# Performance work log

Hardware: AMD Instinct MI355X
Metric: run time of the kernel (lower is better)

## Reference

```python
import jax, jax.numpy as jnp
import numpy as np

# dims: batch, seqlen, d_model, d_inner=2*d_model, d_state, dt_rank=ceil(dm/16), n_layer, vocab, d_conv
B_, L_, DM, DI, N, RK, NL, V, K = 2, 2048, 512, 1024, 16, 32, 4, 32000, 4


def setup_inputs() -> dict:
    key = jax.random.key(0)
    ks = jax.random.split(key, 10)
    s = lambda k, shape, scale: jax.random.normal(k, shape, jnp.float32) * scale
    return {
        "input_ids": jax.random.randint(ks[0], (B_, L_), 0, V),
        "emb": s(ks[1], (V, DM), 0.02),
        "in_proj_w": s(ks[2], (NL, 2 * DI, DM), DM ** -0.5),
        "conv_w": s(ks[3], (NL, DI, K), 0.2),
        "conv_b": jnp.zeros((NL, DI), jnp.float32),
        "x_proj_w": s(ks[4], (NL, RK + 2 * N, DI), DI ** -0.5),
        "dt_proj_w": s(ks[5], (NL, DI, RK), RK ** -0.5),
        "dt_proj_b": jnp.full((NL, DI), -4.6, jnp.float32),  # softplus^-1(~0.01)
        "A_log": jnp.tile(jnp.log(jnp.arange(1, N + 1, dtype=jnp.float32))[None, None, :], (NL, DI, 1)),
        "Dp": jnp.ones((NL, DI), jnp.float32),
        "out_proj_w": s(ks[6], (NL, DM, DI), DI ** -0.5),
        "norm_w": jnp.ones((NL, DM), jnp.float32),
        "norm_b": jnp.zeros((NL, DM), jnp.float32),
        "normf_w": jnp.ones((DM,), jnp.float32),
        "normf_b": jnp.zeros((DM,), jnp.float32),
        "dec_w": s(ks[7], (V, DM), DM ** -0.5),
        "dec_b": jnp.zeros((V,), jnp.float32),
    }


def layer_norm(x, w, b, eps=1e-5):
    m = x.mean(-1, keepdims=True)
    v = ((x - m) ** 2).mean(-1, keepdims=True)
    return (x - m) * jax.lax.rsqrt(v + eps) * w + b


def mamba_mixer(x, iw, cw, cb, xw, dw, db, A_log, Dv, ow):
    B, L, _ = x.shape
    xz = x @ iw.T                      # [B,L,2*DI]
    u, z = jnp.split(xz, 2, -1)
    # depthwise causal conv1d, kernel K
    up = jnp.pad(u, ((0, 0), (K - 1, 0), (0, 0)))
    u = sum(up[:, k:k + L, :] * cw[:, k] for k in range(K)) + cb
    u = jax.nn.silu(u)
    xdbl = u @ xw.T                    # [B,L,RK+2N]
    dt, Bm, Cm = jnp.split(xdbl, [RK, RK + N], -1)
    dt = jax.nn.softplus(dt @ dw.T + db)   # [B,L,DI]
    A = -jnp.exp(A_log)                    # [DI,N]
    dA = jnp.exp(dt[..., None] * A)                              # [B,L,DI,N]
    dBu = dt[..., None] * Bm[:, :, None, :] * u[..., None]       # [B,L,DI,N]

    def step(h, inp):
        dA_t, dBu_t, C_t = inp
        h = dA_t * h + dBu_t
        return h, jnp.einsum('bdn,bn->bd', h, C_t)

    h0 = jnp.zeros((B, DI, N), x.dtype)
    _, ys = jax.lax.scan(step, h0, (dA.transpose(1, 0, 2, 3), dBu.transpose(1, 0, 2, 3), Cm.transpose(1, 0, 2)))
    y = ys.transpose(1, 0, 2) + u * Dv
    y = y * jax.nn.silu(z)
    return y @ ow.T


def reference(input_ids, emb, in_proj_w, conv_w, conv_b, x_proj_w, dt_proj_w, dt_proj_b,
              A_log, Dp, out_proj_w, norm_w, norm_b, normf_w, normf_b, dec_w, dec_b):
    h = emb[input_ids]                 # [B,L,DM]
    residual = None
    for i in range(NL):
        residual = h + residual if residual is not None else h
        hn = layer_norm(residual, norm_w[i], norm_b[i])
        h = mamba_mixer(hn, in_proj_w[i], conv_w[i], conv_b[i], x_proj_w[i],
                        dt_proj_w[i], dt_proj_b[i], A_log[i], Dp[i], out_proj_w[i])
    residual = h + residual
    h = layer_norm(residual, normf_w, normf_b)
    return h @ dec_w.T + dec_b         # [B,L,V]
```

## Files before the change

kernel.cpp:

```cpp
#include <hip/hip_runtime.h>
#include <cstdint>
#include <cstddef>

typedef unsigned short u16;
typedef __attribute__((ext_vector_type(8))) short short8;
typedef __attribute__((ext_vector_type(4))) float f32x4;
typedef __attribute__((ext_vector_type(4))) unsigned short us4;

#define NB 2
#define SEQ 2048
#define DMODEL 512
#define DINNER 1024
#define NSTATE 16
#define RKK 32
#define NLAYER 4
#define VOCAB 32000
#define MROWS 4096
#define NCHUNK 128
#define LCHUNK 16
#define XP_SPLITK 4
#define XP_KCH 256

#define GLOAD16(gp, lp) __builtin_amdgcn_global_load_lds( \
    (const __attribute__((address_space(1))) void*)(gp),  \
    (__attribute__((address_space(3))) void*)(lp), 16, 0, 0)

static __device__ __forceinline__ u16 f2bf(float f) {
  union { float f; uint32_t u; } v; v.f = f;
  uint32_t r = (v.u + 0x7FFFu + ((v.u >> 16) & 1u)) >> 16;
  return (u16)r;
}
static __device__ __forceinline__ float bf2f(u16 x) {
  union { uint32_t u; float f; } v; v.u = ((uint32_t)x) << 16; return v.f;
}

__global__ __launch_bounds__(256) void cvt_all_k(
    const float* __restrict__ ipw, const float* __restrict__ dtw,
    const float* __restrict__ opw, const float* __restrict__ dw,
    const float* __restrict__ xpw,
    u16* __restrict__ w_in, u16* __restrict__ w_dt,
    u16* __restrict__ w_out, u16* __restrict__ w_dec,
    u16* __restrict__ w_xp) {
  const long n0 = (long)NLAYER * 2 * DINNER * DMODEL / 4;
  const long n1 = (long)NLAYER * DINNER * RKK / 4;
  const long n2 = (long)NLAYER * DMODEL * DINNER / 4;
  const long n3 = (long)VOCAB * DMODEL / 4;
  const long n4 = (long)NLAYER * 128 * DINNER / 4;
  long i = (long)blockIdx.x * 256 + threadIdx.x;
  if (i >= n0 + n1 + n2 + n3 + n4) return;
  if (i >= n0 + n1 + n2 + n3) {
    long o4 = (i - n0 - n1 - n2 - n3) * 4;
    int c = (int)(o4 & 1023); int r = ((int)(o4 >> 10)) & 127; int l = (int)(o4 >> 17);
    us4 o;
    if (r < 64) {
      f32x4 v = *(const f32x4*)(xpw + (((long)l * 64 + r) << 10) + c);
      o.x = f2bf(v.x); o.y = f2bf(v.y); o.z = f2bf(v.z); o.w = f2bf(v.w);
    } else { o.x = 0; o.y = 0; o.z = 0; o.w = 0; }
    *(us4*)(w_xp + o4) = o;
    return;
  }
  const float* s; u16* d; long off;
  if (i < n0) { s = ipw; d = w_in; off = i; }
  else if (i < n0 + n1) { s = dtw; d = w_dt; off = i - n0; }
  else if (i < n0 + n1 + n2) { s = opw; d = w_out; off = i - n0 - n1; }
  else { s = dw; d = w_dec; off = i - n0 - n1 - n2; }
  f32x4 v = *(const f32x4*)(s + off * 4);
  us4 o; o.x = f2bf(v.x); o.y = f2bf(v.y); o.z = f2bf(v.z); o.w = f2bf(v.w);
  *(us4*)(d + off * 4) = o;
}

template <int MODE>
__global__ __launch_bounds__(256) void ln_k(const int* __restrict__ ids, const float* __restrict__ emb,
                                            float* __restrict__ resid, const float* __restrict__ h0,
                                            const float* __restrict__ h1,
                                            const float* __restrict__ w, const float* __restrict__ b,
                                            u16* __restrict__ obf) {
  int m = blockIdx.x, t = threadIdx.x;
  long base = (long)m * DMODEL;
  float x0, x1;
  if (MODE == 0) {
    long ebase = (long)ids[m] * DMODEL;
    x0 = emb[ebase + t]; x1 = emb[ebase + t + 256];
    resid[base + t] = x0; resid[base + t + 256] = x1;
  } else {
    x0 = resid[base + t] + h0[base + t] + h1[base + t];
    x1 = resid[base + t + 256] + h0[base + t + 256] + h1[base + t + 256];
    resid[base + t] = x0; resid[base + t + 256] = x1;
  }
  float s = x0 + x1, q = x0 * x0 + x1 * x1;
  #pragma unroll
  for (int o = 1; o < 64; o <<= 1) { s += __shfl_xor(s, o, 64); q += __shfl_xor(q, o, 64); }
  __shared__ float ss[4], qq[4];
  int wv = t >> 6;
  if ((t & 63) == 0) { ss[wv] = s; qq[wv] = q; }
  __syncthreads();
  s = ss[0] + ss[1] + ss[2] + ss[3];
  q = qq[0] + qq[1] + qq[2] + qq[3];
  float mean = s * (1.f / DMODEL);
  float var = q * (1.f / DMODEL) - mean * mean;
  float rs = rsqrtf(var + 1e-5f);
  obf[base + t]       = f2bf((x0 - mean) * rs * w[t] + b[t]);
  obf[base + t + 256] = f2bf((x1 - mean) * rs * w[t + 256] + b[t + 256]);
}

__global__ __launch_bounds__(256) void conv_silu_k(const u16* __restrict__ xzb, const float* __restrict__ cw,
                            const float* __restrict__ cb, u16* __restrict__ ub) {
  int tid = blockIdx.x * 256 + threadIdx.x;
  int d = tid & (DINNER - 1);
  int g = tid >> 10;
  int m0 = g << 3;
  int t0 = m0 & (SEQ - 1);
  float w0 = cw[d * 4 + 0], w1 = cw[d * 4 + 1], w2 = cw[d * 4 + 2], w3 = cw[d * 4 + 3];
  float bias = cb[d];
  float v[11];
  #pragma unroll
  for (int j = 0; j < 11; ++j) {
    int tt = t0 + j - 3;
    v[j] = (tt >= 0) ? bf2f(xzb[(long)(m0 + j - 3) * (2 * DINNER) + d]) : 0.f;
  }
  #pragma unroll
  for (int i = 0; i < 8; ++i) {
    float acc = bias + v[i] * w0 + v[i + 1] * w1 + v[i + 2] * w2 + v[i + 3] * w3;
    float sv = acc / (1.f + __expf(-acc));
    ub[(long)(m0 + i) * DINNER + d] = f2bf(sv);
  }
}

template <int EPI, int BK, bool SPLIT>
__global__ __launch_bounds__(256) void gemm_bf16(
    const u16* __restrict__ A, int lda, const u16* __restrict__ W, int ldw,
    float* __restrict__ C, u16* __restrict__ Cb, int ldc,
    const float* __restrict__ bias, int K, int kchunk, long zstride) {
  const int tid = threadIdx.x;
  const int nwg = gridDim.x * gridDim.y;
  const int wgid = blockIdx.y * gridDim.x + blockIdx.x;
  const int q = nwg >> 3;
  const int swz = (wgid & 7) * q + (wgid >> 3);
  const int bn = swz % gridDim.x, bm = swz / gridDim.x;
  int kb = 0, ke = K;
  if (SPLIT) { kb = blockIdx.z * kchunk; ke = kb + kchunk; C += (long)blockIdx.z * zstride; }
  const int wave = tid >> 6, lane = tid & 63;
  const int wm = (wave >> 1) * 64, wn = (wave & 1) * 64;
  __shared__ __align__(16) u16 sA[128 * BK];
  __shared__ __align__(16) u16 sB[128 * BK];
  f32x4 acc[4][4] = {};
  const long arow0 = (long)bm * 128, brow0 = (long)bn * 128;
  const int frow = lane & 15, fk = (lane >> 4) << 3;
  const int rsw = (frow & 7) << 3;
  for (int k0 = kb; k0 < ke; k0 += BK) {
    __syncthreads();
    if (BK == 32) {
      const int srow = lane >> 2, scol = (lane & 3) << 3;
      #pragma unroll
      for (int i = 0; i < 2; ++i) {
        int c = wave * 2 + i;
        GLOAD16(A + (arow0 + 16 * c + srow) * (long)lda + k0 + scol, sA + c * 512);
        GLOAD16(W + (brow0 + 16 * c + srow) * (long)ldw + k0 + scol, sB + c * 512);
      }
    } else {
      const int srow = lane >> 3;
      const int scol = (((lane & 7) ^ (lane >> 3)) << 3);
      #pragma unroll
      for (int i = 0; i < 4; ++i) {
        int c = wave * 4 + i;
        GLOAD16(A + (arow0 + 8 * c + srow) * (long)lda + k0 + scol, sA + c * 512);
        GLOAD16(W + (brow0 + 8 * c + srow) * (long)ldw + k0 + scol, sB + c * 512);
      }
    }
    asm volatile("s_waitcnt vmcnt(0)" ::: "memory");
    __syncthreads();
    #pragma unroll
    for (int ks = 0; ks < BK / 32; ++ks) {
      short8 aF[4], bF[4];
      #pragma unroll
      for (int i = 0; i < 4; ++i) {
        int idx = (wm + i * 16 + frow) * BK + ks * 32 + fk;
        aF[i] = *(const short8*)(sA + (BK == 64 ? (idx ^ rsw) : idx));
      }
      #pragma unroll
      for (int i = 0; i < 4; ++i) {
        int idx = (wn + i * 16 + frow) * BK + ks * 32 + fk;
        bF[i] = *(const short8*)(sB + (BK == 64 ? (idx ^ rsw) : idx));
      }
      #pragma unroll
      for (int mi = 0; mi < 4; ++mi)
        #pragma unroll
        for (int ni = 0; ni < 4; ++ni)
          acc[mi][ni] = __builtin_amdgcn_mfma_f32_16x16x32_bf16(aF[mi], bF[ni], acc[mi][ni], 0, 0, 0);
    }
  }
  const int ccol = lane & 15, crow = (lane >> 4) << 2;
  #pragma unroll
  for (int mi = 0; mi < 4; ++mi) {
    #pragma unroll
    for (int ni = 0; ni < 4; ++ni) {
      long gr0 = arow0 + wm + mi * 16 + crow;
      long gc = brow0 + wn + ni * 16 + ccol;
      #pragma unroll
      for (int r = 0; r < 4; ++r) {
        float v = acc[mi][ni][r];
        long idx = (gr0 + r) * (long)ldc + gc;
        if (EPI == 0) {
          C[idx] = v;
        } else if (EPI == 1) {
          Cb[idx] = f2bf(v);
        } else if (EPI == 2) {
          float x = v + bias[gc];
          Cb[idx] = f2bf((x > 20.f) ? x : log1pf(__expf(x)));
        } else {
          __builtin_nontemporal_store(v + bias[gc], &C[idx]);
        }
      }
    }
  }
}

__global__ __launch_bounds__(512) void gemm_dec(
    const u16* __restrict__ A, const u16* __restrict__ W,
    float* __restrict__ C, const float* __restrict__ bias) {
  const int tid = threadIdx.x;
  const int nwg = gridDim.x * gridDim.y;
  const int wgid = blockIdx.y * gridDim.x + blockIdx.x;
  const int q = nwg >> 3;
  const int swz = (wgid & 7) * q + (wgid >> 3);
  const int bn = swz % gridDim.x, bm = swz / gridDim.x;
  const int wave = tid >> 6, lane = tid & 63;
  const int wm = (wave >> 1) << 6;
  const int wn = (wave & 1) << 6;
  __shared__ __align__(16) u16 sA[256 * 64];
  __shared__ __align__(16) u16 sB[128 * 64];
  f32x4 acc[4][4] = {};
  const long arow0 = (long)bm * 256, brow0 = (long)bn * 128;
  const int frow = lane & 15, fk = (lane >> 4) << 3;
  const int rsw = (frow & 7) << 3;
  const int srow = lane >> 3;
  const int scol = (((lane & 7) ^ (lane >> 3)) << 3);
  for (int k0 = 0; k0 < DMODEL; k0 += 64) {
    __syncthreads();
    #pragma unroll
    for (int i = 0; i < 4; ++i) {
      int c = wave * 4 + i;
      GLOAD16(A + (arow0 + 8 * c + srow) * (long)DMODEL + k0 + scol, sA + c * 512);
    }
    #pragma unroll
    for (int i = 0; i < 2; ++i) {
      int c = wave * 2 + i;
      GLOAD16(W + (brow0 + 8 * c + srow) * (long)DMODEL + k0 + scol, sB + c * 512);
    }
    asm volatile("s_waitcnt vmcnt(0)" ::: "memory");
    __syncthreads();
    #pragma unroll
    for (int ks = 0; ks < 2; ++ks) {
      short8 aF[4], bF[4];
      #pragma unroll
      for (int i = 0; i < 4; ++i) {
        int idx = (wm + i * 16 + frow) * 64 + ks * 32 + fk;
        aF[i] = *(const short8*)(sA + (idx ^ rsw));
      }
      #pragma unroll
      for (int i = 0; i < 4; ++i) {
        int idx = (wn + i * 16 + frow) * 64 + ks * 32 + fk;
        bF[i] = *(const short8*)(sB + (idx ^ rsw));
      }
      #pragma unroll
      for (int mi = 0; mi < 4; ++mi)
        #pragma unroll
        for (int ni = 0; ni < 4; ++ni)
          acc[mi][ni] = __builtin_amdgcn_mfma_f32_16x16x32_bf16(aF[mi], bF[ni], acc[mi][ni], 0, 0, 0);
    }
  }
  const int ccol = lane & 15, crow = (lane >> 4) << 2;
  #pragma unroll
  for (int mi = 0; mi < 4; ++mi) {
    #pragma unroll
    for (int ni = 0; ni < 4; ++ni) {
      long gr0 = arow0 + wm + mi * 16 + crow;
      long gc = brow0 + wn + ni * 16 + ccol;
      float bv = bias[gc];
      #pragma unroll
      for (int r = 0; r < 4; ++r)
        __builtin_nontemporal_store(acc[mi][ni][r] + bv, &C[(gr0 + r) * (long)VOCAB + gc]);
    }
  }
}

__global__ __launch_bounds__(256) void xp_comb_k(const float* __restrict__ P, float* __restrict__ xd,
                          u16* __restrict__ xdb) {
  long i = (long)blockIdx.x * 256 + threadIdx.x;
  int col = (int)(i & 127);
  if (col >= 64) return;
  float s = 0.f;
  #pragma unroll
  for (int z = 0; z < XP_SPLITK; ++z) s += P[(long)z * MROWS * 128 + i];
  if (col < 32) xdb[i] = f2bf(s);
  else xd[i] = s;
}

__global__ __launch_bounds__(256) void scanA_k(const u16* __restrict__ dtb, const u16* __restrict__ ubf,
                        const float* __restrict__ xd, const float* __restrict__ alog_l,
                        float* __restrict__ P, float* __restrict__ S) {
  int bid = blockIdx.x;
  int tid = threadIdx.x;
  int b = bid >> 9;
  int c = (bid >> 2) & (NCHUNK - 1);
  int d = ((bid & 3) << 8) + tid;
  long rbase = (long)(b * SEQ + c * LCHUNK);
  __shared__ __align__(16) float sB[LCHUNK][NSTATE];
  if (tid < 64) {
    int t = tid >> 2, k4 = (tid & 3) << 2;
    *(f32x4*)&sB[t][k4] = *(const f32x4*)(xd + (rbase + t) * 128 + RKK + k4);
  }
  u16 dtv[LCHUNK], uv[LCHUNK];
  const u16* dp = dtb + rbase * DINNER + d;
  const u16* up = ubf + rbase * DINNER + d;
  #pragma unroll
  for (int tt = 0; tt < LCHUNK; ++tt) { dtv[tt] = dp[(long)tt * DINNER]; uv[tt] = up[(long)tt * DINNER]; }
  float A[NSTATE], h[NSTATE];
  #pragma unroll
  for (int n4 = 0; n4 < 4; ++n4) {
    f32x4 a4 = *(const f32x4*)(alog_l + d * NSTATE + n4 * 4);
    #pragma unroll
    for (int j = 0; j < 4; ++j) { A[n4 * 4 + j] = -__expf(a4[j]); h[n4 * 4 + j] = 0.f; }
  }
  __syncthreads();
  float dsum = 0.f;
  #pragma unroll
  for (int tt = 0; tt < LCHUNK; ++tt) {
    float dv = bf2f(dtv[tt]);
    float du = dv * bf2f(uv[tt]);
    dsum += dv;
    f32x4 b0 = *(const f32x4*)&sB[tt][0], b1 = *(const f32x4*)&sB[tt][4];
    f32x4 b2 = *(const f32x4*)&sB[tt][8], b3 = *(const f32x4*)&sB[tt][12];
    #pragma unroll
    for (int n = 0; n < NSTATE; ++n) {
      float dA = __expf(dv * A[n]);
      float bx = (n < 4) ? b0[n & 3] : (n < 8) ? b1[n & 3] : (n < 12) ? b2[n & 3] : b3[n & 3];
      h[n] = dA * h[n] + du * bx;
    }
  }
  long base = (((long)(b * DINNER + d)) * NCHUNK + c) * NSTATE;
  #pragma unroll
  for (int n4 = 0; n4 < 4; ++n4) {
    f32x4 pv, sv;
    #pragma unroll
    for (int j = 0; j < 4; ++j) { pv[j] = __expf(A[n4 * 4 + j] * dsum); sv[j] = h[n4 * 4 + j]; }
    *(f32x4*)(P + base + n4 * 4) = pv;
    *(f32x4*)(S + base + n4 * 4) = sv;
  }
}

__global__ __launch_bounds__(256) void scanB_k(const float* __restrict__ P, const float* __restrict__ S,
                        float* __restrict__ Hin) {
  int w = blockIdx.x * 4 + (threadIdx.x >> 6);
  int lane = threadIdx.x & 63;
  long base0 = ((long)w * NCHUNK + 2 * lane) * NSTATE;
  long base1 = base0 + NSTATE;
  float p0[NSTATE], s0[NSTATE], p[NSTATE], s[NSTATE];
  #pragma unroll
  for (int n = 0; n < NSTATE; ++n) {
    p0[n] = P[base0 + n]; s0[n] = S[base0 + n];
    float p1 = P[base1 + n], s1 = S[base1 + n];
    p[n] = p1 * p0[n];
    s[n] = p1 * s0[n] + s1;
  }
  #pragma unroll
  for (int off = 1; off < 64; off <<= 1) {
    float pp[NSTATE], sp[NSTATE];
    #pragma unroll
    for (int n = 0; n < NSTATE; ++n) {
      pp[n] = __shfl_up(p[n], off, 64);
      sp[n] = __shfl_up(s[n], off, 64);
    }
    if (lane >= off) {
      #pragma unroll
      for (int n = 0; n < NSTATE; ++n) { s[n] = p[n] * sp[n] + s[n]; p[n] *= pp[n]; }
    }
  }
  #pragma unroll
  for (int n = 0; n < NSTATE; ++n) {
    float hv = __shfl_up(s[n], 1, 64);
    float e = (lane == 0) ? 0.f : hv;
    Hin[base0 + n] = e;
    Hin[base1 + n] = p0[n] * e + s0[n];
  }
}

__global__ __launch_bounds__(256) void scanC_k(const u16* __restrict__ dtb, const u16* __restrict__ ubf,
                        const float* __restrict__ xd, const float* __restrict__ alog_l,
                        const float* __restrict__ Dp_l, const u16* __restrict__ xzb,
                        const float* __restrict__ Hin, u16* __restrict__ ybf) {
  int bid = blockIdx.x;
  int tid = threadIdx.x;
  int b = bid >> 9;
  int c = (bid >> 2) & (NCHUNK - 1);
  int d = ((bid & 3) << 8) + tid;
  long rbase = (long)(b * SEQ + c * LCHUNK);
  __shared__ __align__(16) float sBC[LCHUNK][2 * NSTATE];
  if (tid < 128) {
    int t = tid >> 3, k4 = (tid & 7) << 2;
    *(f32x4*)&sBC[t][k4] = *(const f32x4*)(xd + (rbase + t) * 128 + RKK + k4);
  }
  u16 dtv[LCHUNK], uv[LCHUNK], zv[LCHUNK];
  const u16* dp = dtb + rbase * DINNER + d;
  const u16* up = ubf + rbase * DINNER + d;
  const u16* zp = xzb + rbase * (2 * DINNER) + DINNER + d;
  #pragma unroll
  for (int tt = 0; tt < LCHUNK; ++tt) {
    dtv[tt] = dp[(long)tt * DINNER]; uv[tt] = up[(long)tt * DINNER];
    zv[tt] = zp[(long)tt * 2 * DINNER];
  }
  float A[NSTATE], h[NSTATE];
  long hbase = (((long)(b * DINNER + d)) * NCHUNK + c) * NSTATE;
  #pragma unroll
  for (int n4 = 0; n4 < 4; ++n4) {
    f32x4 a4 = *(const f32x4*)(alog_l + d * NSTATE + n4 * 4);
    f32x4 h4 = *(const f32x4*)(Hin + hbase + n4 * 4);
    #pragma unroll
    for (int j = 0; j < 4; ++j) { A[n4 * 4 + j] = -__expf(a4[j]); h[n4 * 4 + j] = h4[j]; }
  }
  float Dv = Dp_l[d];
  u16* yp = ybf + rbase * DINNER + d;
  __syncthreads();
  #pragma unroll
  for (int tt = 0; tt < LCHUNK; ++tt) {
    float dv = bf2f(dtv[tt]);
    float uvf = bf2f(uv[tt]);
    float du = dv * uvf;
    f32x4 b0 = *(const f32x4*)&sBC[tt][0], b1 = *(const f32x4*)&sBC[tt][4];
    f32x4 b2 = *(const f32x4*)&sBC[tt][8], b3 = *(const f32x4*)&sBC[tt][12];
    f32x4 c0 = *(const f32x4*)&sBC[tt][16], c1 = *(const f32x4*)&sBC[tt][20];
    f32x4 c2 = *(const f32x4*)&sBC[tt][24], c3 = *(const f32x4*)&sBC[tt][28];
    float y = 0.f;
    #pragma unroll
    for (int n = 0; n < NSTATE; ++n) {
      float dA = __expf(dv * A[n]);
      float bx = (n < 4) ? b0[n & 3] : (n < 8) ? b1[n & 3] : (n < 12) ? b2[n & 3] : b3[n & 3];
      float cx = (n < 4) ? c0[n & 3] : (n < 8) ? c1[n & 3] : (n < 12) ? c2[n & 3] : c3[n & 3];
      h[n] = dA * h[n] + du * bx;
      y += h[n] * cx;
    }
    y += uvf * Dv;
    float z = bf2f(zv[tt]);
    y *= z / (1.f + __expf(-z));
    yp[(long)tt * DINNER] = f2bf(y);
  }
}

extern "C" void kernel_launch(void* const* d_in, const int* in_sizes, int n_in,
                              void* d_out, int out_size, void* d_ws, size_t ws_size,
                              hipStream_t stream) {
  (void)in_sizes; (void)n_in; (void)out_size; (void)ws_size;
  const int*   ids = (const int*)d_in[0];
  const float* emb = (const float*)d_in[1];
  const float* ipw = (const float*)d_in[2];
  const float* cw  = (const float*)d_in[3];
  const float* cb  = (const float*)d_in[4];
  const float* xpw = (const float*)d_in[5];
  const float* dtw = (const float*)d_in[6];
  const float* dtb = (const float*)d_in[7];
  const float* alg = (const float*)d_in[8];
  const float* Dpp = (const float*)d_in[9];
  const float* opw = (const float*)d_in[10];
  const float* nw  = (const float*)d_in[11];
  const float* nb  = (const float*)d_in[12];
  const float* nfw = (const float*)d_in[13];
  const float* nfb = (const float*)d_in[14];
  const float* dw  = (const float*)d_in[15];
  const float* db  = (const float*)d_in[16];

  char* p = (char*)d_ws;
  auto carve = [&](size_t bytes) { void* r = (void*)p; p += (bytes + 255) & ~(size_t)255; return r; };
  float* resid  = (float*)carve((size_t)MROWS * DMODEL * 4);
  float* hmixP  = (float*)carve((size_t)2 * MROWS * DMODEL * 4);
  u16*   hnbf   = (u16*)  carve((size_t)MROWS * DMODEL * 2);
  u16*   hfbf   = (u16*)  carve((size_t)MROWS * DMODEL * 2);
  u16*   xzb    = (u16*)  carve((size_t)MROWS * 2 * DINNER * 2);
  u16*   ubf    = (u16*)  carve((size_t)MROWS * DINNER * 2);
  float* xdbl   = (float*)carve((size_t)MROWS * 128 * 4);
  u16*   xdblbf = (u16*)  carve((size_t)MROWS * 128 * 2);
  float* xdP    = (float*)carve((size_t)XP_SPLITK * MROWS * 128 * 4);
  u16*   dtb16  = (u16*)  carve((size_t)MROWS * DINNER * 2);
  u16*   ybf    = (u16*)  carve((size_t)MROWS * DINNER * 2);
  float* chkP   = (float*)carve((size_t)NB * DINNER * NCHUNK * NSTATE * 4);
  float* chkS   = (float*)carve((size_t)NB * DINNER * NCHUNK * NSTATE * 4);
  float* hin    = (float*)carve((size_t)NB * DINNER * NCHUNK * NSTATE * 4);
  u16*   w_in   = (u16*)carve((size_t)NLAYER * 2 * DINNER * DMODEL * 2);
  u16*   w_xp   = (u16*)carve((size_t)NLAYER * 128 * DINNER * 2);
  u16*   w_dt   = (u16*)carve((size_t)NLAYER * DINNER * RKK * 2);
  u16*   w_out  = (u16*)carve((size_t)NLAYER * DMODEL * DINNER * 2);
  u16*   w_dec  = (u16*)carve((size_t)VOCAB * DMODEL * 2);

  {
    long nv = ((long)NLAYER * 2 * DINNER * DMODEL + (long)NLAYER * DINNER * RKK +
               (long)NLAYER * DMODEL * DINNER + (long)VOCAB * DMODEL +
               (long)NLAYER * 128 * DINNER) / 4;
    cvt_all_k<<<(int)((nv + 255) / 256), 256, 0, stream>>>(
        ipw, dtw, opw, dw, xpw, w_in, w_dt, w_out, w_dec, w_xp);
  }

  for (int i = 0; i < NLAYER; ++i) {
    if (i == 0)
      ln_k<0><<<MROWS, 256, 0, stream>>>(ids, emb, resid, nullptr, nullptr, nw, nb, hnbf);
    else
      ln_k<1><<<MROWS, 256, 0, stream>>>(nullptr, nullptr, resid, hmixP, hmixP + (long)MROWS * DMODEL,
                                         nw + i * DMODEL, nb + i * DMODEL, hnbf);
    gemm_bf16<1, 64, false><<<dim3(2 * DINNER / 128, MROWS / 128), 256, 0, stream>>>(
        hnbf, DMODEL, w_in + (long)i * 2 * DINNER * DMODEL, DMODEL,
        nullptr, xzb, 2 * DINNER, nullptr, DMODEL, 0, 0);
    conv_silu_k<<<(MROWS / 8 * DINNER) / 256, 256, 0, stream>>>(
        xzb, cw + (long)i * DINNER * 4, cb + i * DINNER, ubf);
    gemm_bf16<0, 64, true><<<dim3(1, MROWS / 128, XP_SPLITK), 256, 0, stream>>>(
        ubf, DINNER, w_xp + (long)i * 128 * DINNER, DINNER,
        xdP, nullptr, 128, nullptr, DINNER, XP_KCH, (long)MROWS * 128);
    xp_comb_k<<<(MROWS * 128) / 256, 256, 0, stream>>>(xdP, xdbl, xdblbf);
    gemm_bf16<2, 32, false><<<dim3(DINNER / 128, MROWS / 128), 256, 0, stream>>>(
        xdblbf, 128, w_dt + (long)i * DINNER * RKK, RKK,
        nullptr, dtb16, DINNER, dtb + i * DINNER, RKK, 0, 0);
    scanA_k<<<NB * NCHUNK * 4, 256, 0, stream>>>(
        dtb16, ubf, xdbl, alg + (long)i * DINNER * NSTATE, chkP, chkS);
    scanB_k<<<(NB * DINNER) / 4, 256, 0, stream>>>(chkP, chkS, hin);
    scanC_k<<<NB * NCHUNK * 4, 256, 0, stream>>>(
        dtb16, ubf, xdbl, alg + (long)i * DINNER * NSTATE, Dpp + i * DINNER, xzb, hin, ybf);
    gemm_bf16<0, 64, true><<<dim3(DMODEL / 128, MROWS / 128, 2), 256, 0, stream>>>(
        ybf, DINNER, w_out + (long)i * DMODEL * DINNER, DINNER,
        hmixP, nullptr, DMODEL, nullptr, DINNER, DINNER / 2, (long)MROWS * DMODEL);
  }
  ln_k<1><<<MROWS, 256, 0, stream>>>(nullptr, nullptr, resid, hmixP, hmixP + (long)MROWS * DMODEL,
                                     nfw, nfb, hfbf);
  gemm_dec<<<dim3(VOCAB / 128, MROWS / 256), 512, 0, stream>>>(
      hfbf, w_dec, (float*)d_out, db);
}
```

Measured before the change: 827.7 us.

## Double-buffer decoder GEMM, lengthen scan chunks, raise split-K for projections

The decoder GEMM now uses double-buffered shared-memory tiles with K-step 32, prefetching the next tile while MFMAs run on the current one instead of load-wait-compute per step. The scan moves to 64 chunks of 32 steps, so the cross-chunk combine in scanB handles one chunk per lane instead of pairing two. The x_proj split-K rises to 8 and out_proj split-K to 4, with the layer norm summing the extra partial buffers. This adds parallelism for the small GEMMs but costs more partial-sum traffic and longer sequential scan chunks.

Result: faster. 774.6 us (-6.4%).

```diff
diff --git a/kernel.cpp b/kernel.cpp
--- a/kernel.cpp
+++ b/kernel.cpp
@@ -16,10 +16,11 @@
 #define NLAYER 4
 #define VOCAB 32000
 #define MROWS 4096
-#define NCHUNK 128
-#define LCHUNK 16
-#define XP_SPLITK 4
-#define XP_KCH 256
+#define NCHUNK 64
+#define LCHUNK 32
+#define XP_SPLITK 8
+#define XP_KCH 128
+#define OUT_SPLITK 4
 
 #define GLOAD16(gp, lp) __builtin_amdgcn_global_load_lds( \
     (const __attribute__((address_space(1))) void*)(gp),  \
@@ -71,8 +72,8 @@
 
 template <int MODE>
 __global__ __launch_bounds__(256) void ln_k(const int* __restrict__ ids, const float* __restrict__ emb,
-                                            float* __restrict__ resid, const float* __restrict__ h0,
-                                            const float* __restrict__ h1,
+                                            float* __restrict__ resid, const float* __restrict__ hP,
+                                            long pstride,
                                             const float* __restrict__ w, const float* __restrict__ b,
                                             u16* __restrict__ obf) {
   int m = blockIdx.x, t = threadIdx.x;
@@ -83,8 +84,13 @@
     x0 = emb[ebase + t]; x1 = emb[ebase + t + 256];
     resid[base + t] = x0; resid[base + t + 256] = x1;
   } else {
-    x0 = resid[base + t] + h0[base + t] + h1[base + t];
-    x1 = resid[base + t + 256] + h0[base + t + 256] + h1[base + t + 256];
+    x0 = resid[base + t];
+    x1 = resid[base + t + 256];
+    #pragma unroll
+    for (int z = 0; z < OUT_SPLITK; ++z) {
+      x0 += hP[z * pstride + base + t];
+      x1 += hP[z * pstride + base + t + 256];
+    }
     resid[base + t] = x0; resid[base + t + 256] = x1;
   }
   float s = x0 + x1, q = x0 * x0 + x1 * x1;
@@ -227,47 +233,51 @@
   const int wave = tid >> 6, lane = tid & 63;
   const int wm = (wave >> 1) << 6;
   const int wn = (wave & 1) << 6;
-  __shared__ __align__(16) u16 sA[256 * 64];
-  __shared__ __align__(16) u16 sB[128 * 64];
+  __shared__ __align__(16) u16 sA[2][256 * 32];
+  __shared__ __align__(16) u16 sB[2][128 * 32];
   f32x4 acc[4][4] = {};
   const long arow0 = (long)bm * 256, brow0 = (long)bn * 128;
   const int frow = lane & 15, fk = (lane >> 4) << 3;
-  const int rsw = (frow & 7) << 3;
-  const int srow = lane >> 3;
-  const int scol = (((lane & 7) ^ (lane >> 3)) << 3);
-  for (int k0 = 0; k0 < DMODEL; k0 += 64) {
-    __syncthreads();
+  const int srow = lane >> 2;
+  const int scol = (((lane & 3) ^ (srow & 3)) << 3);
+  #pragma unroll
+  for (int i = 0; i < 2; ++i) {
+    int c = wave * 2 + i;
+    GLOAD16(A + (arow0 + 16 * c + srow) * (long)DMODEL + scol, sA[0] + c * 512);
+  }
+  GLOAD16(W + (brow0 + 16 * wave + srow) * (long)DMODEL + scol, sB[0] + wave * 512);
+  asm volatile("s_waitcnt vmcnt(0)" ::: "memory");
+  __syncthreads();
+  int cur = 0;
+  for (int k0 = 0; k0 < DMODEL; k0 += 32) {
+    if (k0 + 32 < DMODEL) {
+      int nb = cur ^ 1;
+      #pragma unroll
+      for (int i = 0; i < 2; ++i) {
+        int c = wave * 2 + i;
+        GLOAD16(A + (arow0 + 16 * c + srow) * (long)DMODEL + k0 + 32 + scol, sA[nb] + c * 512);
+      }
+      GLOAD16(W + (brow0 + 16 * wave + srow) * (long)DMODEL + k0 + 32 + scol, sB[nb] + wave * 512);
+    }
+    short8 aF[4], bF[4];
     #pragma unroll
     for (int i = 0; i < 4; ++i) {
-      int c = wave * 4 + i;
-      GLOAD16(A + (arow0 + 8 * c + srow) * (long)DMODEL + k0 + scol, sA + c * 512);
-    }
-    #pragma unroll
-    for (int i = 0; i < 2; ++i) {
-      int c = wave * 2 + i;
-      GLOAD16(W + (brow0 + 8 * c + srow) * (long)DMODEL + k0 + scol, sB + c * 512);
-    }
+      int row = wm + i * 16 + frow;
+      aF[i] = *(const short8*)(sA[cur] + ((row * 32 + fk) ^ ((row & 3) << 3)));
+    }
+    #pragma unroll
+    for (int i = 0; i < 4; ++i) {
+      int row = wn + i * 16 + frow;
+      bF[i] = *(const short8*)(sB[cur] + ((row * 32 + fk) ^ ((row & 3) << 3)));
+    }
+    #pragma unroll
+    for (int mi = 0; mi < 4; ++mi)
+      #pragma unroll
+      for (int ni = 0; ni < 4; ++ni)
+        acc[mi][ni] = __builtin_amdgcn_mfma_f32_16x16x32_bf16(aF[mi], bF[ni], acc[mi][ni], 0, 0, 0);
     asm volatile("s_waitcnt vmcnt(0)" ::: "memory");
     __syncthreads();
-    #pragma unroll
-    for (int ks = 0; ks < 2; ++ks) {
-      short8 aF[4], bF[4];
-      #pragma unroll
-      for (int i = 0; i < 4; ++i) {
-        int idx = (wm + i * 16 + frow) * 64 + ks * 32 + fk;
-        aF[i] = *(const short8*)(sA + (idx ^ rsw));
-      }
-      #pragma unroll
-      for (int i = 0; i < 4; ++i) {
-        int idx = (wn + i * 16 + frow) * 64 + ks * 32 + fk;
-        bF[i] = *(const short8*)(sB + (idx ^ rsw));
-      }
-      #pragma unroll
-      for (int mi = 0; mi < 4; ++mi)
-        #pragma unroll
-        for (int ni = 0; ni < 4; ++ni)
-          acc[mi][ni] = __builtin_amdgcn_mfma_f32_16x16x32_bf16(aF[mi], bF[ni], acc[mi][ni], 0, 0, 0);
-    }
+    cur ^= 1;
   }
   const int ccol = lane & 15, crow = (lane >> 4) << 2;
   #pragma unroll
@@ -301,12 +311,12 @@
                         float* __restrict__ P, float* __restrict__ S) {
   int bid = blockIdx.x;
   int tid = threadIdx.x;
-  int b = bid >> 9;
+  int b = bid >> 8;
   int c = (bid >> 2) & (NCHUNK - 1);
   int d = ((bid & 3) << 8) + tid;
   long rbase = (long)(b * SEQ + c * LCHUNK);
   __shared__ __align__(16) float sB[LCHUNK][NSTATE];
-  if (tid < 64) {
+  if (tid < 128) {
     int t = tid >> 2, k4 = (tid & 3) << 2;
     *(f32x4*)&sB[t][k4] = *(const f32x4*)(xd + (rbase + t) * 128 + RKK + k4);
   }
@@ -353,16 +363,10 @@
                         float* __restrict__ Hin) {
   int w = blockIdx.x * 4 + (threadIdx.x >> 6);
   int lane = threadIdx.x & 63;
-  long base0 = ((long)w * NCHUNK + 2 * lane) * NSTATE;
-  long base1 = base0 + NSTATE;
-  float p0[NSTATE], s0[NSTATE], p[NSTATE], s[NSTATE];
-  #pragma unroll
-  for (int n = 0; n < NSTATE; ++n) {
-    p0[n] = P[base0 + n]; s0[n] = S[base0 + n];
-    float p1 = P[base1 + n], s1 = S[base1 + n];
-    p[n] = p1 * p0[n];
-    s[n] = p1 * s0[n] + s1;
-  }
+  long base = ((long)w * NCHUNK + lane) * NSTATE;
+  float p[NSTATE], s[NSTATE];
+  #pragma unroll
+  for (int n = 0; n < NSTATE; ++n) { p[n] = P[base + n]; s[n] = S[base + n]; }
   #pragma unroll
   for (int off = 1; off < 64; off <<= 1) {
     float pp[NSTATE], sp[NSTATE];
@@ -379,9 +383,7 @@
   #pragma unroll
   for (int n = 0; n < NSTATE; ++n) {
     float hv = __shfl_up(s[n], 1, 64);
-    float e = (lane == 0) ? 0.f : hv;
-    Hin[base0 + n] = e;
-    Hin[base1 + n] = p0[n] * e + s0[n];
+    Hin[base + n] = (lane == 0) ? 0.f : hv;
   }
 }
 
@@ -391,12 +393,12 @@
                         const float* __restrict__ Hin, u16* __restrict__ ybf) {
   int bid = blockIdx.x;
   int tid = threadIdx.x;
-  int b = bid >> 9;
+  int b = bid >> 8;
   int c = (bid >> 2) & (NCHUNK - 1);
   int d = ((bid & 3) << 8) + tid;
   long rbase = (long)(b * SEQ + c * LCHUNK);
   __shared__ __align__(16) float sBC[LCHUNK][2 * NSTATE];
-  if (tid < 128) {
+  {
     int t = tid >> 3, k4 = (tid & 7) << 2;
     *(f32x4*)&sBC[t][k4] = *(const f32x4*)(xd + (rbase + t) * 128 + RKK + k4);
   }
@@ -471,7 +473,7 @@
   char* p = (char*)d_ws;
   auto carve = [&](size_t bytes) { void* r = (void*)p; p += (bytes + 255) & ~(size_t)255; return r; };
   float* resid  = (float*)carve((size_t)MROWS * DMODEL * 4);
-  float* hmixP  = (float*)carve((size_t)2 * MROWS * DMODEL * 4);
+  float* hmixP  = (float*)carve((size_t)OUT_SPLITK * MROWS * DMODEL * 4);
   u16*   hnbf   = (u16*)  carve((size_t)MROWS * DMODEL * 2);
   u16*   hfbf   = (u16*)  carve((size_t)MROWS * DMODEL * 2);
   u16*   xzb    = (u16*)  carve((size_t)MROWS * 2 * DINNER * 2);
@@ -500,9 +502,9 @@
 
   for (int i = 0; i < NLAYER; ++i) {
     if (i == 0)
-      ln_k<0><<<MROWS, 256, 0, stream>>>(ids, emb, resid, nullptr, nullptr, nw, nb, hnbf);
+      ln_k<0><<<MROWS, 256, 0, stream>>>(ids, emb, resid, nullptr, 0, nw, nb, hnbf);
     else
-      ln_k<1><<<MROWS, 256, 0, stream>>>(nullptr, nullptr, resid, hmixP, hmixP + (long)MROWS * DMODEL,
+      ln_k<1><<<MROWS, 256, 0, stream>>>(nullptr, nullptr, resid, hmixP, (long)MROWS * DMODEL,
                                          nw + i * DMODEL, nb + i * DMODEL, hnbf);
     gemm_bf16<1, 64, false><<<dim3(2 * DINNER / 128, MROWS / 128), 256, 0, stream>>>(
         hnbf, DMODEL, w_in + (long)i * 2 * DINNER * DMODEL, DMODEL,
@@ -521,11 +523,11 @@
     scanB_k<<<(NB * DINNER) / 4, 256, 0, stream>>>(chkP, chkS, hin);
     scanC_k<<<NB * NCHUNK * 4, 256, 0, stream>>>(
         dtb16, ubf, xdbl, alg + (long)i * DINNER * NSTATE, Dpp + i * DINNER, xzb, hin, ybf);
-    gemm_bf16<0, 64, true><<<dim3(DMODEL / 128, MROWS / 128, 2), 256, 0, stream>>>(
+    gemm_bf16<0, 64, true><<<dim3(DMODEL / 128, MROWS / 128, OUT_SPLITK), 256, 0, stream>>>(
         ybf, DINNER, w_out + (long)i * DMODEL * DINNER, DINNER,
-        hmixP, nullptr, DMODEL, nullptr, DINNER, DINNER / 2, (long)MROWS * DMODEL);
-  }
-  ln_k<1><<<MROWS, 256, 0, stream>>>(nullptr, nullptr, resid, hmixP, hmixP + (long)MROWS * DMODEL,
+        hmixP, nullptr, DMODEL, nullptr, DINNER, DINNER / OUT_SPLITK, (long)MROWS * DMODEL);
+  }
+  ln_k<1><<<MROWS, 256, 0, stream>>>(nullptr, nullptr, resid, hmixP, (long)MROWS * DMODEL,
                                      nfw, nfb, hfbf);
   gemm_dec<<<dim3(VOCAB / 128, MROWS / 256), 512, 0, stream>>>(
       hfbf, w_dec, (float*)d_out, db);
```
